# Performance work log

Measured on AMD Instinct MI355X. Metric: run time of the kernel, lower is better.

The kernel has to match this reference:

```python
import jax, jax.numpy as jnp
import numpy as np

N_NODES = 256
COND = 64
ARCH = [256, 512, 1024]
E = N_NODES * (N_NODES - 1) // 2  # 32640 upper-triangular edges
OUT = 2 * E                        # 65280 final-layer width
B = 512
CUTOFF = 0.0
TAU = 1.0


def _make_params(key, dims):
    ws, bs = [], []
    for i, (din, dout) in enumerate(zip(dims[:-1], dims[1:])):
        k = jax.random.fold_in(key, i)
        kw, kb = jax.random.split(k)
        ws.append(jax.random.normal(kw, (din, dout), jnp.float32) * 0.02)
        bs.append(jax.random.normal(kb, (dout,), jnp.float32) * 0.02)
    return ws, bs


def setup_inputs() -> dict:
    key = jax.random.key(0)
    kx, kg, kbig, ksmall = jax.random.split(key, 4)
    x = jax.random.normal(kx, (B, COND), jnp.float32)
    gumbel = jax.random.gumbel(kg, (B, E, 2), jnp.float32)
    dims = [COND] + ARCH + [OUT]
    bw, bb = _make_params(kbig, dims)
    sw, sb = _make_params(ksmall, dims)
    inp = {"x": x, "gumbel": gumbel}
    for i in range(4):
        inp[f"bw{i}"] = bw[i]; inp[f"bb{i}"] = bb[i]
        inp[f"sw{i}"] = sw[i]; inp[f"sb{i}"] = sb[i]
    return inp


def _expert_adj(x, ws, bs, gumbel):
    # MLP: relu on all but last layer
    h = x
    for w, b in zip(ws[:-1], bs[:-1]):
        h = jax.nn.relu(h @ w + b)
    logits = (h @ ws[-1] + bs[-1]).reshape(x.shape[0], E, 2)
    # hard gumbel-softmax (straight-through), tau=1
    g = (logits + gumbel) / TAU
    y_soft = jax.nn.softmax(g, axis=-1)
    y_hard = jax.nn.one_hot(jnp.argmax(g, axis=-1), 2, dtype=y_soft.dtype)
    y = y_hard + y_soft - jax.lax.stop_gradient(y_soft)
    x0 = y[:, :, 0]  # [B, E]
    iu, ju = jnp.triu_indices(N_NODES, k=1)
    adj = jnp.zeros((x.shape[0], N_NODES, N_NODES), x0.dtype)
    adj = adj.at[:, iu, ju].set(x0)
    return adj + jnp.swapaxes(adj, 1, 2)


def reference(x, gumbel,
              bw0, bb0, bw1, bb1, bw2, bb2, bw3, bb3,
              sw0, sb0, sw1, sb1, sw2, sb2, sw3, sb3):
    big_ws, big_bs = [bw0, bw1, bw2, bw3], [bb0, bb1, bb2, bb3]
    small_ws, small_bs = [sw0, sw1, sw2, sw3], [sb0, sb1, sb2, sb3]
    adj_big = _expert_adj(x, big_ws, big_bs, gumbel)
    adj_small = _expert_adj(x, small_ws, small_bs, gumbel)
    mask_big = x[:, 0] > CUTOFF  # [B]
    out = jnp.where(mask_big[:, None, None], adj_big, adj_small)
    return out
```

## Files before the change

kernel.cpp:

```cpp
#include <hip/hip_runtime.h>

#define N_NODES 256
#define COND    64
#define E_PAIRS 32640
#define OUTCOLS 65280
#define BATCH   512
#define SLOTS   576
#define D1      256
#define D2      512
#define D3      1024

__global__ void k0_sort(const float* __restrict__ x, int* __restrict__ meta,
                        int* __restrict__ borig) {
    __shared__ int mask[BATCH];
    __shared__ int bor[SLOTS];
    int t = threadIdx.x;
    if (t < SLOTS) bor[t] = -1;
    if (t < BATCH) mask[t] = (x[t * COND] > 0.0f) ? 1 : 0;
    __syncthreads();
    if (t == 0) {
        int nbig = 0;
        for (int b = 0; b < BATCH; ++b) nbig += mask[b];
        int S = (nbig + 63) & ~63;
        int ib = 0, is = S;
        for (int b = 0; b < BATCH; ++b) {
            if (mask[b]) bor[ib++] = b; else bor[is++] = b;
        }
        meta[0] = S;
    }
    __syncthreads();
    if (t < SLOTS) borig[t] = bor[t];
}

__global__ __launch_bounds__(256) void k1_mlp(
    const float* __restrict__ x,
    const float* __restrict__ bw0, const float* __restrict__ bb0,
    const float* __restrict__ sw0, const float* __restrict__ sb0,
    const float* __restrict__ bw1, const float* __restrict__ bb1,
    const float* __restrict__ sw1, const float* __restrict__ sb1,
    const float* __restrict__ bw2, const float* __restrict__ bb2,
    const float* __restrict__ sw2, const float* __restrict__ sb2,
    const int* __restrict__ borig, float* __restrict__ hbuf) {
    __shared__ float xs[COND];
    __shared__ float h1[D1];
    __shared__ float h2[D2];
    int s = blockIdx.x, t = threadIdx.x;
    int b = borig[s];
    if (b < 0) {
        for (int c = t; c < D3; c += 256) hbuf[s * D3 + c] = 0.0f;
        return;
    }
    bool big = x[b * COND] > 0.0f;
    const float* w0 = big ? bw0 : sw0;  const float* b0 = big ? bb0 : sb0;
    const float* w1 = big ? bw1 : sw1;  const float* b1 = big ? bb1 : sb1;
    const float* w2 = big ? bw2 : sw2;  const float* b2 = big ? bb2 : sb2;
    if (t < COND) xs[t] = x[b * COND + t];
    __syncthreads();
    {
        float acc = 0.f;
        #pragma unroll 8
        for (int k = 0; k < COND; ++k) acc = fmaf(xs[k], w0[k * D1 + t], acc);
        h1[t] = fmaxf(acc + b0[t], 0.f);
    }
    __syncthreads();
    {
        float a0 = 0.f, a1 = 0.f;
        #pragma unroll 4
        for (int k = 0; k < D1; ++k) {
            float hv = h1[k];
            a0 = fmaf(hv, w1[k * D2 + t], a0);
            a1 = fmaf(hv, w1[k * D2 + t + 256], a1);
        }
        h2[t]       = fmaxf(a0 + b1[t], 0.f);
        h2[t + 256] = fmaxf(a1 + b1[t + 256], 0.f);
    }
    __syncthreads();
    {
        float a0 = 0.f, a1 = 0.f, a2 = 0.f, a3 = 0.f;
        #pragma unroll 4
        for (int k = 0; k < D2; ++k) {
            float hv = h2[k];
            a0 = fmaf(hv, w2[k * D3 + t], a0);
            a1 = fmaf(hv, w2[k * D3 + t + 256], a1);
            a2 = fmaf(hv, w2[k * D3 + t + 512], a2);
            a3 = fmaf(hv, w2[k * D3 + t + 768], a3);
        }
        hbuf[s * D3 + t]       = fmaxf(a0 + b2[t], 0.f);
        hbuf[s * D3 + t + 256] = fmaxf(a1 + b2[t + 256], 0.f);
        hbuf[s * D3 + t + 512] = fmaxf(a2 + b2[t + 512], 0.f);
        hbuf[s * D3 + t + 768] = fmaxf(a3 + b2[t + 768], 0.f);
    }
}

#define BM   64
#define BNW  256
#define BND  128
#define BK   16
__global__ __launch_bounds__(256) void k2_logits(
    const float* __restrict__ hbuf,
    const float* __restrict__ bw3, const float* __restrict__ bb3,
    const float* __restrict__ sw3, const float* __restrict__ sb3,
    const float* __restrict__ gum,
    const int* __restrict__ meta, const int* __restrict__ borig,
    unsigned char* __restrict__ bits) {
    __shared__ float hs[BK][BM + 4];
    __shared__ float wt[BK][BND + 4];
    int tid = threadIdx.x;
    int by = blockIdx.x;
    int bx = blockIdx.y;
    int r0 = by * BM;
    int cb = bx * BNW;
    int S = meta[0];
    bool big = (r0 < S);
    const float* w3 = big ? bw3 : sw3;
    const float* b3 = big ? bb3 : sb3;

    int lm  = tid >> 2;
    int lq  = tid & 3;
    int wk  = tid >> 4;
    int wc  = (tid & 15) * 16;
    int wd  = (tid & 15) * 8;

    int tm = tid >> 5;
    int tn = tid & 31;

    float acc[8][4];
    #pragma unroll
    for (int i = 0; i < 8; ++i)
        #pragma unroll
        for (int j = 0; j < 4; ++j) acc[i][j] = 0.f;

    for (int k0 = 0; k0 < D3; k0 += BK) {
        float4 hv = *(const float4*)&hbuf[(size_t)(r0 + lm) * D3 + k0 + lq * 4];
        const float* wrow = &w3[(size_t)(k0 + wk) * OUTCOLS + cb + wc];
        float4 wv0 = *(const float4*)&wrow[0];
        float4 wv1 = *(const float4*)&wrow[4];
        float4 wv2 = *(const float4*)&wrow[8];
        float4 wv3 = *(const float4*)&wrow[12];
        __syncthreads();
        hs[lq * 4 + 0][lm] = hv.x;
        hs[lq * 4 + 1][lm] = hv.y;
        hs[lq * 4 + 2][lm] = hv.z;
        hs[lq * 4 + 3][lm] = hv.w;
        float4 d0, d1;
        d0.x = wv0.x - wv0.y;  d0.y = wv0.z - wv0.w;
        d0.z = wv1.x - wv1.y;  d0.w = wv1.z - wv1.w;
        d1.x = wv2.x - wv2.y;  d1.y = wv2.z - wv2.w;
        d1.z = wv3.x - wv3.y;  d1.w = wv3.z - wv3.w;
        *(float4*)&wt[wk][wd]     = d0;
        *(float4*)&wt[wk][wd + 4] = d1;
        __syncthreads();
        #pragma unroll
        for (int kk = 0; kk < BK; ++kk) {
            float4 a0 = *(const float4*)&hs[kk][tm * 8];
            float4 a1 = *(const float4*)&hs[kk][tm * 8 + 4];
            float4 bf = *(const float4*)&wt[kk][tn * 4];
            float am[8] = {a0.x, a0.y, a0.z, a0.w, a1.x, a1.y, a1.z, a1.w};
            float bn[4] = {bf.x, bf.y, bf.z, bf.w};
            #pragma unroll
            for (int i = 0; i < 8; ++i)
                #pragma unroll
                for (int j = 0; j < 4; ++j)
                    acc[i][j] = fmaf(am[i], bn[j], acc[i][j]);
        }
    }

    float4 bv0 = *(const float4*)&b3[cb + tn * 8];
    float4 bv1 = *(const float4*)&b3[cb + tn * 8 + 4];
    float bd0 = bv0.x - bv0.y;
    float bd1 = bv0.z - bv0.w;
    float bd2 = bv1.x - bv1.y;
    float bd3 = bv1.z - bv1.w;
    int ebase = bx * BND + tn * 4;
    #pragma unroll
    for (int i = 0; i < 8; ++i) {
        int slot = r0 + tm * 8 + i;
        int b = borig[slot];
        if (b < 0) continue;
        const float* gp = &gum[(size_t)b * OUTCOLS + (size_t)ebase * 2];
        float4 gv0 = *(const float4*)&gp[0];
        float4 gv1 = *(const float4*)&gp[4];
        uchar4 v;
        v.x = ((acc[i][0] + bd0) + (gv0.x - gv0.y) >= 0.f) ? 1 : 0;
        v.y = ((acc[i][1] + bd1) + (gv0.z - gv0.w) >= 0.f) ? 1 : 0;
        v.z = ((acc[i][2] + bd2) + (gv1.x - gv1.y) >= 0.f) ? 1 : 0;
        v.w = ((acc[i][3] + bd3) + (gv1.z - gv1.w) >= 0.f) ? 1 : 0;
        *(uchar4*)&bits[(size_t)b * E_PAIRS + ebase] = v;
    }
}

__global__ __launch_bounds__(256) void k3_expand(
    const unsigned char* __restrict__ bits, float* __restrict__ out) {
    __shared__ unsigned char L[64][68];
    const int ti_tab[10] = {0,0,0,0,1,1,1,2,2,3};
    const int tj_tab[10] = {0,1,2,3,1,2,3,2,3,3};
    int p = blockIdx.x;
    int b = blockIdx.y;
    int ti = ti_tab[p], tj = tj_tab[p];
    int t = threadIdx.x;

    {
        int r = t >> 2;
        int q = t & 3;
        int i = ti * 64 + r;
        long base = (long)b * E_PAIRS + (long)i * (511 - i) / 2 - i - 1;
        int j0 = tj * 64 + q * 16;
        #pragma unroll
        for (int k = 0; k < 16; ++k) {
            int j = j0 + k;
            unsigned char v = (j > i) ? bits[base + j] : (unsigned char)0;
            L[r][q * 16 + k] = v;
        }
    }
    __syncthreads();

    int h  = t >> 4;
    int w4 = (t & 15) * 4;

    {
        #pragma unroll
        for (int rr = 0; rr < 4; ++rr) {
            int ii = rr * 16 + h;
            int i_ = ti * 64 + ii;
            float4 v;
            if (ti == tj) {
                int jj;
                jj = w4 + 0; v.x = (jj > ii) ? (float)L[ii][jj] : (jj < ii ? (float)L[jj][ii] : 0.f);
                jj = w4 + 1; v.y = (jj > ii) ? (float)L[ii][jj] : (jj < ii ? (float)L[jj][ii] : 0.f);
                jj = w4 + 2; v.z = (jj > ii) ? (float)L[ii][jj] : (jj < ii ? (float)L[jj][ii] : 0.f);
                jj = w4 + 3; v.w = (jj > ii) ? (float)L[ii][jj] : (jj < ii ? (float)L[jj][ii] : 0.f);
            } else {
                v.x = (float)L[ii][w4 + 0];
                v.y = (float)L[ii][w4 + 1];
                v.z = (float)L[ii][w4 + 2];
                v.w = (float)L[ii][w4 + 3];
            }
            size_t o = (((size_t)b * 256 + i_) * 256) + tj * 64 + w4;
            *(float4*)&out[o] = v;
        }
    }

    if (ti != tj) {
        #pragma unroll
        for (int rr = 0; rr < 4; ++rr) {
            int jj = rr * 16 + h;
            int j_ = tj * 64 + jj;
            float4 v;
            v.x = (float)L[w4 + 0][jj];
            v.y = (float)L[w4 + 1][jj];
            v.z = (float)L[w4 + 2][jj];
            v.w = (float)L[w4 + 3][jj];
            size_t o = (((size_t)b * 256 + j_) * 256) + ti * 64 + w4;
            *(float4*)&out[o] = v;
        }
    }
}

extern "C" void kernel_launch(void* const* d_in, const int* in_sizes, int n_in,
                              void* d_out, int out_size, void* d_ws, size_t ws_size,
                              hipStream_t stream) {
    const float* x   = (const float*)d_in[0];
    const float* gum = (const float*)d_in[1];
    const float* bw0 = (const float*)d_in[2];  const float* bb0 = (const float*)d_in[3];
    const float* sw0 = (const float*)d_in[4];  const float* sb0 = (const float*)d_in[5];
    const float* bw1 = (const float*)d_in[6];  const float* bb1 = (const float*)d_in[7];
    const float* sw1 = (const float*)d_in[8];  const float* sb1 = (const float*)d_in[9];
    const float* bw2 = (const float*)d_in[10]; const float* bb2 = (const float*)d_in[11];
    const float* sw2 = (const float*)d_in[12]; const float* sb2 = (const float*)d_in[13];
    const float* bw3 = (const float*)d_in[14]; const float* bb3 = (const float*)d_in[15];
    const float* sw3 = (const float*)d_in[16]; const float* sb3 = (const float*)d_in[17];

    char* ws = (char*)d_ws;
    int*   meta  = (int*)ws;
    int*   borig = (int*)(ws + 64);
    float* hbuf  = (float*)(ws + 4096);
    unsigned char* bits = (unsigned char*)(ws + 4096 + (size_t)SLOTS * D3 * 4);
    float* out = (float*)d_out;

    k0_sort<<<1, SLOTS, 0, stream>>>(x, meta, borig);
    k1_mlp<<<SLOTS, 256, 0, stream>>>(x, bw0, bb0, sw0, sb0, bw1, bb1, sw1, sb1,
                                      bw2, bb2, sw2, sb2, borig, hbuf);
    k2_logits<<<dim3(9, 255), 256, 0, stream>>>(hbuf, bw3, bb3, sw3, sb3, gum,
                                                meta, borig, bits);
    k3_expand<<<dim3(10, BATCH), 256, 0, stream>>>(bits, out);
}
```

Before: 1.099 ms.

## Prefetch next K-tile in logits GEMM and use square bit layout for expand

The logits GEMM loop now loads the next K-tile from global memory into registers before running the FMA loop on the current shared tile, overlapping load latency with compute, and the FMA body is written out explicitly. When the workspace is large enough, decisions are written into a padded 256x256 byte matrix per batch row, with the start (i,j) computed via a sqrt inversion. The expand kernel can then read each tile row with one vector load instead of guarded byte loads. This costs extra workspace and turns k2's output into scattered byte stores.

Result: slower. 1.136 ms (+3.3%).

```diff
diff --git a/kernel.cpp b/kernel.cpp
--- a/kernel.cpp
+++ b/kernel.cpp
@@ -96,6 +96,14 @@
 #define BNW  256
 #define BND  128
 #define BK   16
+
+#define FMA_ROW(r, a) \
+    acc[r][0] = fmaf(a, bf.x, acc[r][0]); \
+    acc[r][1] = fmaf(a, bf.y, acc[r][1]); \
+    acc[r][2] = fmaf(a, bf.z, acc[r][2]); \
+    acc[r][3] = fmaf(a, bf.w, acc[r][3]);
+
+template <bool SQ>
 __global__ __launch_bounds__(256) void k2_logits(
     const float* __restrict__ hbuf,
     const float* __restrict__ bw3, const float* __restrict__ bb3,
@@ -130,39 +138,55 @@
         #pragma unroll
         for (int j = 0; j < 4; ++j) acc[i][j] = 0.f;
 
-    for (int k0 = 0; k0 < D3; k0 += BK) {
-        float4 hv = *(const float4*)&hbuf[(size_t)(r0 + lm) * D3 + k0 + lq * 4];
-        const float* wrow = &w3[(size_t)(k0 + wk) * OUTCOLS + cb + wc];
-        float4 wv0 = *(const float4*)&wrow[0];
-        float4 wv1 = *(const float4*)&wrow[4];
-        float4 wv2 = *(const float4*)&wrow[8];
-        float4 wv3 = *(const float4*)&wrow[12];
+    const float* hrow = &hbuf[(size_t)(r0 + lm) * D3 + lq * 4];
+    float4 hv = *(const float4*)hrow;
+    const float* wrow = &w3[(size_t)wk * OUTCOLS + cb + wc];
+    float4 wv0 = *(const float4*)&wrow[0];
+    float4 wv1 = *(const float4*)&wrow[4];
+    float4 wv2 = *(const float4*)&wrow[8];
+    float4 wv3 = *(const float4*)&wrow[12];
+
+    for (int k0 = 0;;) {
         __syncthreads();
         hs[lq * 4 + 0][lm] = hv.x;
         hs[lq * 4 + 1][lm] = hv.y;
         hs[lq * 4 + 2][lm] = hv.z;
         hs[lq * 4 + 3][lm] = hv.w;
-        float4 d0, d1;
-        d0.x = wv0.x - wv0.y;  d0.y = wv0.z - wv0.w;
-        d0.z = wv1.x - wv1.y;  d0.w = wv1.z - wv1.w;
-        d1.x = wv2.x - wv2.y;  d1.y = wv2.z - wv2.w;
-        d1.z = wv3.x - wv3.y;  d1.w = wv3.z - wv3.w;
-        *(float4*)&wt[wk][wd]     = d0;
-        *(float4*)&wt[wk][wd + 4] = d1;
+        {
+            float4 d0, d1;
+            d0.x = wv0.x - wv0.y;  d0.y = wv0.z - wv0.w;
+            d0.z = wv1.x - wv1.y;  d0.w = wv1.z - wv1.w;
+            d1.x = wv2.x - wv2.y;  d1.y = wv2.z - wv2.w;
+            d1.z = wv3.x - wv3.y;  d1.w = wv3.z - wv3.w;
+            *(float4*)&wt[wk][wd]     = d0;
+            *(float4*)&wt[wk][wd + 4] = d1;
+        }
         __syncthreads();
+        k0 += BK;
+        bool more = (k0 < D3);
+        if (more) {
+            hv = *(const float4*)&hrow[k0];
+            const float* wr = &wrow[(size_t)k0 * OUTCOLS];
+            wv0 = *(const float4*)&wr[0];
+            wv1 = *(const float4*)&wr[4];
+            wv2 = *(const float4*)&wr[8];
+            wv3 = *(const float4*)&wr[12];
+        }
         #pragma unroll
         for (int kk = 0; kk < BK; ++kk) {
             float4 a0 = *(const float4*)&hs[kk][tm * 8];
             float4 a1 = *(const float4*)&hs[kk][tm * 8 + 4];
             float4 bf = *(const float4*)&wt[kk][tn * 4];
-            float am[8] = {a0.x, a0.y, a0.z, a0.w, a1.x, a1.y, a1.z, a1.w};
-            float bn[4] = {bf.x, bf.y, bf.z, bf.w};
-            #pragma unroll
-            for (int i = 0; i < 8; ++i)
-                #pragma unroll
-                for (int j = 0; j < 4; ++j)
-                    acc[i][j] = fmaf(am[i], bn[j], acc[i][j]);
-        }
+            FMA_ROW(0, a0.x)
+            FMA_ROW(1, a0.y)
+            FMA_ROW(2, a0.z)
+            FMA_ROW(3, a0.w)
+            FMA_ROW(4, a1.x)
+            FMA_ROW(5, a1.y)
+            FMA_ROW(6, a1.z)
+            FMA_ROW(7, a1.w)
+        }
+        if (!more) break;
     }
 
     float4 bv0 = *(const float4*)&b3[cb + tn * 8];
@@ -172,6 +196,16 @@
     float bd2 = bv1.x - bv1.y;
     float bd3 = bv1.z - bv1.w;
     int ebase = bx * BND + tn * 4;
+
+    int i0 = 0, j0 = 0;
+    if (SQ) {
+        float fe = 65280.25f - 2.0f * (float)ebase;
+        i0 = (int)(255.5f - sqrtf(fe));
+        if (i0 * (511 - i0) / 2 > ebase) --i0;
+        if ((i0 + 1) * (510 - i0) / 2 <= ebase) ++i0;
+        j0 = ebase - i0 * (511 - i0) / 2 + i0 + 1;
+    }
+
     #pragma unroll
     for (int i = 0; i < 8; ++i) {
         int slot = r0 + tm * 8 + i;
@@ -180,16 +214,29 @@
         const float* gp = &gum[(size_t)b * OUTCOLS + (size_t)ebase * 2];
         float4 gv0 = *(const float4*)&gp[0];
         float4 gv1 = *(const float4*)&gp[4];
-        uchar4 v;
-        v.x = ((acc[i][0] + bd0) + (gv0.x - gv0.y) >= 0.f) ? 1 : 0;
-        v.y = ((acc[i][1] + bd1) + (gv0.z - gv0.w) >= 0.f) ? 1 : 0;
-        v.z = ((acc[i][2] + bd2) + (gv1.x - gv1.y) >= 0.f) ? 1 : 0;
-        v.w = ((acc[i][3] + bd3) + (gv1.z - gv1.w) >= 0.f) ? 1 : 0;
-        *(uchar4*)&bits[(size_t)b * E_PAIRS + ebase] = v;
-    }
-}
-
-__global__ __launch_bounds__(256) void k3_expand(
+        unsigned char c0 = ((acc[i][0] + bd0) + (gv0.x - gv0.y) >= 0.f) ? 1 : 0;
+        unsigned char c1 = ((acc[i][1] + bd1) + (gv0.z - gv0.w) >= 0.f) ? 1 : 0;
+        unsigned char c2 = ((acc[i][2] + bd2) + (gv1.x - gv1.y) >= 0.f) ? 1 : 0;
+        unsigned char c3 = ((acc[i][3] + bd3) + (gv1.z - gv1.w) >= 0.f) ? 1 : 0;
+        if (SQ) {
+            size_t rowb = ((size_t)b << 16);
+            int ii = i0, jj = j0;
+            bits[rowb + ((size_t)ii << 8) + jj] = c0;
+            if (++jj == 256) { ++ii; jj = ii + 1; }
+            bits[rowb + ((size_t)ii << 8) + jj] = c1;
+            if (++jj == 256) { ++ii; jj = ii + 1; }
+            bits[rowb + ((size_t)ii << 8) + jj] = c2;
+            if (++jj == 256) { ++ii; jj = ii + 1; }
+            bits[rowb + ((size_t)ii << 8) + jj] = c3;
+        } else {
+            uchar4 v;
+            v.x = c0; v.y = c1; v.z = c2; v.w = c3;
+            *(uchar4*)&bits[(size_t)b * E_PAIRS + ebase] = v;
+        }
+    }
+}
+
+__global__ __launch_bounds__(256) void k3_expand_sq(
     const unsigned char* __restrict__ bits, float* __restrict__ out) {
     __shared__ unsigned char L[64][68];
     const int ti_tab[10] = {0,0,0,0,1,1,1,2,2,3};
@@ -203,14 +250,12 @@
         int r = t >> 2;
         int q = t & 3;
         int i = ti * 64 + r;
-        long base = (long)b * E_PAIRS + (long)i * (511 - i) / 2 - i - 1;
-        int j0 = tj * 64 + q * 16;
-        #pragma unroll
-        for (int k = 0; k < 16; ++k) {
-            int j = j0 + k;
-            unsigned char v = (j > i) ? bits[base + j] : (unsigned char)0;
-            L[r][q * 16 + k] = v;
-        }
+        const unsigned char* src = &bits[(((size_t)b << 8) + i) * 256 + tj * 64 + q * 16];
+        uint4 v = *(const uint4*)src;
+        *(unsigned int*)&L[r][q * 16 + 0]  = v.x;
+        *(unsigned int*)&L[r][q * 16 + 4]  = v.y;
+        *(unsigned int*)&L[r][q * 16 + 8]  = v.z;
+        *(unsigned int*)&L[r][q * 16 + 12] = v.w;
     }
     __syncthreads();
 
@@ -256,6 +301,70 @@
     }
 }
 
+__global__ __launch_bounds__(256) void k3_expand(
+    const unsigned char* __restrict__ bits, float* __restrict__ out) {
+    __shared__ unsigned char L[64][68];
+    const int ti_tab[10] = {0,0,0,0,1,1,1,2,2,3};
+    const int tj_tab[10] = {0,1,2,3,1,2,3,2,3,3};
+    int p = blockIdx.x;
+    int b = blockIdx.y;
+    int ti = ti_tab[p], tj = tj_tab[p];
+    int t = threadIdx.x;
+    {
+        int r = t >> 2;
+        int q = t & 3;
+        int i = ti * 64 + r;
+        long base = (long)b * E_PAIRS + (long)i * (511 - i) / 2 - i - 1;
+        int j0 = tj * 64 + q * 16;
+        #pragma unroll
+        for (int k = 0; k < 16; ++k) {
+            int j = j0 + k;
+            unsigned char v = (j > i) ? bits[base + j] : (unsigned char)0;
+            L[r][q * 16 + k] = v;
+        }
+    }
+    __syncthreads();
+
+    int h  = t >> 4;
+    int w4 = (t & 15) * 4;
+    {
+        #pragma unroll
+        for (int rr = 0; rr < 4; ++rr) {
+            int ii = rr * 16 + h;
+            int i_ = ti * 64 + ii;
+            float4 v;
+            if (ti == tj) {
+                int jj;
+                jj = w4 + 0; v.x = (jj > ii) ? (float)L[ii][jj] : (jj < ii ? (float)L[jj][ii] : 0.f);
+                jj = w4 + 1; v.y = (jj > ii) ? (float)L[ii][jj] : (jj < ii ? (float)L[jj][ii] : 0.f);
+                jj = w4 + 2; v.z = (jj > ii) ? (float)L[ii][jj] : (jj < ii ? (float)L[jj][ii] : 0.f);
+                jj = w4 + 3; v.w = (jj > ii) ? (float)L[ii][jj] : (jj < ii ? (float)L[jj][ii] : 0.f);
+            } else {
+                v.x = (float)L[ii][w4 + 0];
+                v.y = (float)L[ii][w4 + 1];
+                v.z = (float)L[ii][w4 + 2];
+                v.w = (float)L[ii][w4 + 3];
+            }
+            size_t o = (((size_t)b * 256 + i_) * 256) + tj * 64 + w4;
+            *(float4*)&out[o] = v;
+        }
+    }
+    if (ti != tj) {
+        #pragma unroll
+        for (int rr = 0; rr < 4; ++rr) {
+            int jj = rr * 16 + h;
+            int j_ = tj * 64 + jj;
+            float4 v;
+            v.x = (float)L[w4 + 0][jj];
+            v.y = (float)L[w4 + 1][jj];
+            v.z = (float)L[w4 + 2][jj];
+            v.w = (float)L[w4 + 3][jj];
+            size_t o = (((size_t)b * 256 + j_) * 256) + ti * 64 + w4;
+            *(float4*)&out[o] = v;
+        }
+    }
+}
+
 extern "C" void kernel_launch(void* const* d_in, const int* in_sizes, int n_in,
                               void* d_out, int out_size, void* d_ws, size_t ws_size,
                               hipStream_t stream) {
@@ -277,10 +386,19 @@
     unsigned char* bits = (unsigned char*)(ws + 4096 + (size_t)SLOTS * D3 * 4);
     float* out = (float*)d_out;
 
+    size_t need_sq = 4096 + (size_t)SLOTS * D3 * 4 + (size_t)BATCH * 65536;
+    bool sq = (ws_size >= need_sq);
+
     k0_sort<<<1, SLOTS, 0, stream>>>(x, meta, borig);
     k1_mlp<<<SLOTS, 256, 0, stream>>>(x, bw0, bb0, sw0, sb0, bw1, bb1, sw1, sb1,
                                       bw2, bb2, sw2, sb2, borig, hbuf);
-    k2_logits<<<dim3(9, 255), 256, 0, stream>>>(hbuf, bw3, bb3, sw3, sb3, gum,
-                                                meta, borig, bits);
-    k3_expand<<<dim3(10, BATCH), 256, 0, stream>>>(bits, out);
-}
+    if (sq) {
+        k2_logits<true><<<dim3(9, 255), 256, 0, stream>>>(hbuf, bw3, bb3, sw3, sb3,
+                                                          gum, meta, borig, bits);
+        k3_expand_sq<<<dim3(10, BATCH), 256, 0, stream>>>(bits, out);
+    } else {
+        k2_logits<false><<<dim3(9, 255), 256, 0, stream>>>(hbuf, bw3, bb3, sw3, sb3,
+                                                           gum, meta, borig, bits);
+        k3_expand<<<dim3(10, BATCH), 256, 0, stream>>>(bits, out);
+    }
+}
```

## Replace per-row MLP kernel with tiled GEMM layers and ballot-based sort

Applied to the files above, without the earlier changes.

The single-row-per-block MLP kernel, which re-read each weight matrix for every batch row, is replaced by three launches of a templated 64x64 register-tiled GEMM with shared-memory staging. The launches run over the expert-sorted slots, so each weight tile is reused across 64 rows. The serial single-thread partition in the sort kernel becomes a wave-ballot prefix count. This adds two extra launches and intermediate activation buffers in exchange for far less redundant weight traffic.

Result: faster. 1.078 ms (-2.0%).

```diff
diff --git a/kernel.cpp b/kernel.cpp
--- a/kernel.cpp
+++ b/kernel.cpp
@@ -12,83 +12,117 @@
 
 __global__ void k0_sort(const float* __restrict__ x, int* __restrict__ meta,
                         int* __restrict__ borig) {
-    __shared__ int mask[BATCH];
-    __shared__ int bor[SLOTS];
+    __shared__ int wc[9];
     int t = threadIdx.x;
-    if (t < SLOTS) bor[t] = -1;
-    if (t < BATCH) mask[t] = (x[t * COND] > 0.0f) ? 1 : 0;
+    if (t < SLOTS) borig[t] = -1;
+    int m = 0;
+    if (t < BATCH) m = (x[t * COND] > 0.0f) ? 1 : 0;
+    unsigned long long bm = __ballot(m);
+    int wave = t >> 6;
+    int lane = t & 63;
+    int lanePre = __popcll(bm & ((1ull << lane) - 1ull));
+    if (lane == 0) wc[wave] = __popcll(bm);
     __syncthreads();
-    if (t == 0) {
-        int nbig = 0;
-        for (int b = 0; b < BATCH; ++b) nbig += mask[b];
-        int S = (nbig + 63) & ~63;
-        int ib = 0, is = S;
-        for (int b = 0; b < BATCH; ++b) {
-            if (mask[b]) bor[ib++] = b; else bor[is++] = b;
-        }
-        meta[0] = S;
-    }
-    __syncthreads();
-    if (t < SLOTS) borig[t] = bor[t];
-}
-
-__global__ __launch_bounds__(256) void k1_mlp(
-    const float* __restrict__ x,
-    const float* __restrict__ bw0, const float* __restrict__ bb0,
-    const float* __restrict__ sw0, const float* __restrict__ sb0,
-    const float* __restrict__ bw1, const float* __restrict__ bb1,
-    const float* __restrict__ sw1, const float* __restrict__ sb1,
-    const float* __restrict__ bw2, const float* __restrict__ bb2,
-    const float* __restrict__ sw2, const float* __restrict__ sb2,
-    const int* __restrict__ borig, float* __restrict__ hbuf) {
-    __shared__ float xs[COND];
-    __shared__ float h1[D1];
-    __shared__ float h2[D2];
-    int s = blockIdx.x, t = threadIdx.x;
-    int b = borig[s];
-    if (b < 0) {
-        for (int c = t; c < D3; c += 256) hbuf[s * D3 + c] = 0.0f;
-        return;
-    }
-    bool big = x[b * COND] > 0.0f;
-    const float* w0 = big ? bw0 : sw0;  const float* b0 = big ? bb0 : sb0;
-    const float* w1 = big ? bw1 : sw1;  const float* b1 = big ? bb1 : sb1;
-    const float* w2 = big ? bw2 : sw2;  const float* b2 = big ? bb2 : sb2;
-    if (t < COND) xs[t] = x[b * COND + t];
-    __syncthreads();
-    {
-        float acc = 0.f;
-        #pragma unroll 8
-        for (int k = 0; k < COND; ++k) acc = fmaf(xs[k], w0[k * D1 + t], acc);
-        h1[t] = fmaxf(acc + b0[t], 0.f);
-    }
-    __syncthreads();
-    {
-        float a0 = 0.f, a1 = 0.f;
-        #pragma unroll 4
-        for (int k = 0; k < D1; ++k) {
-            float hv = h1[k];
-            a0 = fmaf(hv, w1[k * D2 + t], a0);
-            a1 = fmaf(hv, w1[k * D2 + t + 256], a1);
-        }
-        h2[t]       = fmaxf(a0 + b1[t], 0.f);
-        h2[t + 256] = fmaxf(a1 + b1[t + 256], 0.f);
-    }
-    __syncthreads();
-    {
-        float a0 = 0.f, a1 = 0.f, a2 = 0.f, a3 = 0.f;
-        #pragma unroll 4
-        for (int k = 0; k < D2; ++k) {
-            float hv = h2[k];
-            a0 = fmaf(hv, w2[k * D3 + t], a0);
-            a1 = fmaf(hv, w2[k * D3 + t + 256], a1);
-            a2 = fmaf(hv, w2[k * D3 + t + 512], a2);
-            a3 = fmaf(hv, w2[k * D3 + t + 768], a3);
-        }
-        hbuf[s * D3 + t]       = fmaxf(a0 + b2[t], 0.f);
-        hbuf[s * D3 + t + 256] = fmaxf(a1 + b2[t + 256], 0.f);
-        hbuf[s * D3 + t + 512] = fmaxf(a2 + b2[t + 512], 0.f);
-        hbuf[s * D3 + t + 768] = fmaxf(a3 + b2[t + 768], 0.f);
+    int nbig = 0, preBig = 0;
+    #pragma unroll
+    for (int w = 0; w < 8; ++w) {
+        int c = wc[w];
+        if (w < wave) preBig += c;
+        nbig += c;
+    }
+    int S = (nbig + 63) & ~63;
+    if (t < BATCH) {
+        int onesBefore = preBig + lanePre;
+        int slot = m ? onesBefore : (S + (t - onesBefore));
+        borig[slot] = t;
+    }
+    if (t == 0) meta[0] = S;
+}
+
+template <bool GATHER, int K, int DOUT>
+__global__ __launch_bounds__(256) void k1_gemm(
+    const float* __restrict__ in,
+    const float* __restrict__ wbig, const float* __restrict__ bbig,
+    const float* __restrict__ wsml, const float* __restrict__ bsml,
+    const int* __restrict__ meta, const int* __restrict__ borig,
+    float* __restrict__ out) {
+    __shared__ float hs[16][64 + 4];
+    __shared__ float wt[16][64 + 4];
+    int tid = threadIdx.x;
+    int by = blockIdx.x;
+    int bx = blockIdx.y;
+    int r0 = by * 64;
+    int cb = bx * 64;
+    int S = meta[0];
+    bool big = (r0 < S);
+    const float* w = big ? wbig : wsml;
+    const float* bias = big ? bbig : bsml;
+
+    int lm = tid >> 2;
+    int lq = tid & 3;
+    int wk = tid >> 4;
+    int wc = (tid & 15) * 4;
+
+    int tm = tid >> 4;
+    int tn = tid & 15;
+
+    const float* hrow;
+    if (GATHER) {
+        int b = borig[r0 + lm];
+        hrow = (b >= 0) ? &in[(size_t)b * K] : (const float*)0;
+    } else {
+        hrow = &in[(size_t)(r0 + lm) * K];
+    }
+
+    float acc[4][4];
+    #pragma unroll
+    for (int i = 0; i < 4; ++i)
+        #pragma unroll
+        for (int j = 0; j < 4; ++j) acc[i][j] = 0.f;
+
+    for (int k0 = 0; k0 < K; k0 += 16) {
+        float4 hv = make_float4(0.f, 0.f, 0.f, 0.f);
+        if (!GATHER || hrow) hv = *(const float4*)&hrow[k0 + lq * 4];
+        float4 wv = *(const float4*)&w[(size_t)(k0 + wk) * DOUT + cb + wc];
+        __syncthreads();
+        hs[lq * 4 + 0][lm] = hv.x;
+        hs[lq * 4 + 1][lm] = hv.y;
+        hs[lq * 4 + 2][lm] = hv.z;
+        hs[lq * 4 + 3][lm] = hv.w;
+        *(float4*)&wt[wk][wc] = wv;
+        __syncthreads();
+        #pragma unroll
+        for (int kk = 0; kk < 16; ++kk) {
+            float4 a  = *(const float4*)&hs[kk][tm * 4];
+            float4 bf = *(const float4*)&wt[kk][tn * 4];
+            acc[0][0] = fmaf(a.x, bf.x, acc[0][0]);
+            acc[0][1] = fmaf(a.x, bf.y, acc[0][1]);
+            acc[0][2] = fmaf(a.x, bf.z, acc[0][2]);
+            acc[0][3] = fmaf(a.x, bf.w, acc[0][3]);
+            acc[1][0] = fmaf(a.y, bf.x, acc[1][0]);
+            acc[1][1] = fmaf(a.y, bf.y, acc[1][1]);
+            acc[1][2] = fmaf(a.y, bf.z, acc[1][2]);
+            acc[1][3] = fmaf(a.y, bf.w, acc[1][3]);
+            acc[2][0] = fmaf(a.z, bf.x, acc[2][0]);
+            acc[2][1] = fmaf(a.z, bf.y, acc[2][1]);
+            acc[2][2] = fmaf(a.z, bf.z, acc[2][2]);
+            acc[2][3] = fmaf(a.z, bf.w, acc[2][3]);
+            acc[3][0] = fmaf(a.w, bf.x, acc[3][0]);
+            acc[3][1] = fmaf(a.w, bf.y, acc[3][1]);
+            acc[3][2] = fmaf(a.w, bf.z, acc[3][2]);
+            acc[3][3] = fmaf(a.w, bf.w, acc[3][3]);
+        }
+    }
+
+    float4 bv = *(const float4*)&bias[cb + tn * 4];
+    #pragma unroll
+    for (int i = 0; i < 4; ++i) {
+        float4 o;
+        o.x = fmaxf(acc[i][0] + bv.x, 0.f);
+        o.y = fmaxf(acc[i][1] + bv.y, 0.f);
+        o.z = fmaxf(acc[i][2] + bv.z, 0.f);
+        o.w = fmaxf(acc[i][3] + bv.w, 0.f);
+        *(float4*)&out[(size_t)(r0 + tm * 4 + i) * DOUT + cb + tn * 4] = o;
     }
 }
 
@@ -273,13 +307,19 @@
     char* ws = (char*)d_ws;
     int*   meta  = (int*)ws;
     int*   borig = (int*)(ws + 64);
-    float* hbuf  = (float*)(ws + 4096);
-    unsigned char* bits = (unsigned char*)(ws + 4096 + (size_t)SLOTS * D3 * 4);
+    float* act1  = (float*)(ws + 4096);
+    float* act2  = (float*)(ws + 4096 + 589824);
+    float* hbuf  = (float*)(ws + 4096 + 589824 + 1179648);
+    unsigned char* bits = (unsigned char*)(ws + 4194304);
     float* out = (float*)d_out;
 
     k0_sort<<<1, SLOTS, 0, stream>>>(x, meta, borig);
-    k1_mlp<<<SLOTS, 256, 0, stream>>>(x, bw0, bb0, sw0, sb0, bw1, bb1, sw1, sb1,
-                                      bw2, bb2, sw2, sb2, borig, hbuf);
+    k1_gemm<true,  COND, D1><<<dim3(9, D1 / 64), 256, 0, stream>>>(
+        x,    bw0, bb0, sw0, sb0, meta, borig, act1);
+    k1_gemm<false, D1,   D2><<<dim3(9, D2 / 64), 256, 0, stream>>>(
+        act1, bw1, bb1, sw1, sb1, meta, borig, act2);
+    k1_gemm<false, D2,   D3><<<dim3(9, D3 / 64), 256, 0, stream>>>(
+        act2, bw2, bb2, sw2, sb2, meta, borig, hbuf);
     k2_logits<<<dim3(9, 255), 256, 0, stream>>>(hbuf, bw3, bb3, sw3, sb3, gum,
                                                 meta, borig, bits);
     k3_expand<<<dim3(10, BATCH), 256, 0, stream>>>(bits, out);
```
